# Optimization experiments

Hardware: AMD Instinct MI355X
Metric: run time of the kernel (lower is better)

Reference implementation:

```python
import jax, jax.numpy as jnp
import numpy as np

N_NODES = 1_000_000
N_EDGES = 16_000_000
N_IN, HID, N_OUT = 128, 32, 16


def setup_inputs() -> dict:
    key = jax.random.key(0)
    ks = jax.random.split(key, 8)
    x = jax.random.normal(ks[0], (N_NODES, N_IN), dtype=jnp.float32)
    edge_index = jax.random.randint(ks[1], (2, N_EDGES), 0, N_NODES, dtype=jnp.int64)
    edge_weight = jax.random.uniform(ks[2], (N_EDGES,), dtype=jnp.float32)
    # ChebConv(K=1) parameters: one linear per layer + bias
    def glorot(k, fan_in, fan_out):
        s = jnp.sqrt(6.0 / (fan_in + fan_out))
        return jax.random.uniform(k, (fan_in, fan_out), minval=-s, maxval=s, dtype=jnp.float32)
    W0 = glorot(ks[3], N_IN, HID)
    b0 = jnp.zeros((HID,), dtype=jnp.float32)
    W1 = glorot(ks[4], HID, HID)
    b1 = jnp.zeros((HID,), dtype=jnp.float32)
    W2 = glorot(ks[5], HID, N_OUT)
    b2 = jnp.zeros((N_OUT,), dtype=jnp.float32)
    return {"x": x, "edge_index": edge_index, "edge_weight": edge_weight,
            "W0": W0, "b0": b0, "W1": W1, "b1": b1, "W2": W2, "b2": b2}


def reference(x, edge_index, edge_weight, W0, b0, W1, b1, W2, b2):
    # PyG ChebConv with K=1: out = lins[0](Tx_0) + bias, Tx_0 = x.
    # The Laplacian propagation over edge_index/edge_weight is only used for K>=2,
    # so edge_index/edge_weight do not enter the math (kept for signature fidelity).
    h = jax.nn.relu(x @ W0 + b0)      # ChebConv1 + relu
    h = jax.nn.relu(h @ W1 + b1)      # ChebConv2 + relu
    # Dropout(p=0.0) is identity
    return h @ W2 + b2                # ChebConv3 -> [N, nOutputs]
```

## Files before the change

### kernel.cpp

```cpp
#include <hip/hip_runtime.h>


#define N_IN  128
#define HID   32
#define N_OUT 16

using f32x4  = __attribute__((ext_vector_type(4))) float;
using short8 = __attribute__((ext_vector_type(8))) short;
using uint4v = __attribute__((ext_vector_type(4))) unsigned int;

#define N_CHUNKS 22
#define TOTAL_WF_SHORTS (N_CHUNKS * 512)
#define WLDS_GRANULES (N_CHUNKS * 64)

__device__ __forceinline__ unsigned fu(float f) {
    union { float f; unsigned u; } v; v.f = f; return v.u;
}
__device__ __forceinline__ float uf(unsigned u) {
    union { unsigned u; float f; } v; v.u = u; return v.f;
}
__device__ __forceinline__ unsigned short f2bf_rne(float f) {
    unsigned u = fu(f);
    return (unsigned short)((u + 0x7fffu + ((u >> 16) & 1u)) >> 16);
}

__global__ void split_weights(const float* __restrict__ W0,
                              const float* __restrict__ W1,
                              const float* __restrict__ W2,
                              unsigned short* __restrict__ wf) {
    int idx = blockIdx.x * blockDim.x + threadIdx.x;
    if (idx >= TOTAL_WF_SHORTS) return;
    int chunk  = idx >> 9;
    int within = idx & 511;
    int lane = within >> 3;
    int j    = within & 7;
    const float* W; int ncol, k, col, hl;
    if (chunk < 16) {
        int kc = chunk >> 2, nh = (chunk >> 1) & 1; hl = chunk & 1;
        k = kc * 32 + 8 * (lane >> 4) + j; col = nh * 16 + (lane & 15);
        W = W0; ncol = HID;
    } else if (chunk < 20) {
        int c2 = chunk - 16, nh = c2 >> 1; hl = c2 & 1;
        k = 8 * (lane >> 4) + j; col = nh * 16 + (lane & 15);
        W = W1; ncol = HID;
    } else {
        hl = chunk - 20;
        k = 8 * (lane >> 4) + j; col = lane & 15;
        W = W2; ncol = N_OUT;
    }
    float v = W[k * ncol + col];
    unsigned hi_bits = fu(v) & 0xFFFF0000u;
    wf[idx] = (hl == 0) ? (unsigned short)(hi_bits >> 16)
                        : f2bf_rne(v - uf(hi_bits));
}

#define MFMA3(acc, ah, al, bh, bl)                                          \
    do {                                                                    \
        acc = __builtin_amdgcn_mfma_f32_16x16x32_bf16(ah, bh, acc, 0, 0, 0);\
        acc = __builtin_amdgcn_mfma_f32_16x16x32_bf16(al, bh, acc, 0, 0, 0);\
        acc = __builtin_amdgcn_mfma_f32_16x16x32_bf16(ah, bl, acc, 0, 0, 0);\
    } while (0)

__global__ __launch_bounds__(256, 4) void gnn_mfma(
    const float* __restrict__ x, const unsigned short* __restrict__ wf,
    const float* __restrict__ b0, const float* __restrict__ b1,
    const float* __restrict__ b2, float* __restrict__ out,
    int n_tiles, int stride)
{
    __shared__ __align__(16) unsigned short wlds[N_CHUNKS * 512];
    __shared__ __align__(16) unsigned short hbuf[4][2][16][40];

    const int tid  = threadIdx.x;
    const int wave = tid >> 6;
    const int l    = tid & 63;
    const int r16  = l & 15;
    const int g    = l >> 4;

    {
        const uint4v* wfv = reinterpret_cast<const uint4v*>(wf);
        uint4v* wl = reinterpret_cast<uint4v*>(wlds);
        for (int gg = tid; gg < WLDS_GRANULES; gg += 256)
            wl[gg] = wfv[gg];
    }
    __syncthreads();

    const short8* WL = reinterpret_cast<const short8*>(wlds);

    const float bc0a = b0[r16], bc0b = b0[16 + r16];
    const float bc1a = b1[r16], bc1b = b1[16 + r16];
    const float bc2  = b2[r16];

    const int gw = blockIdx.x * 4 + wave;

    for (int tile = gw; tile < n_tiles; tile += stride) {
        const int nb = tile * 16;

        f32x4 acc0 = {0.f, 0.f, 0.f, 0.f};
        f32x4 acc1 = {0.f, 0.f, 0.f, 0.f};
        const float* xrow = x + (size_t)(nb + r16) * N_IN + g * 8;

        #pragma unroll
        for (int kc = 0; kc < 4; ++kc) {
            f32x4 xa = __builtin_nontemporal_load(
                reinterpret_cast<const f32x4*>(xrow + kc * 32));
            f32x4 xb = __builtin_nontemporal_load(
                reinterpret_cast<const f32x4*>(xrow + kc * 32 + 4));
            float f[8] = {xa[0], xa[1], xa[2], xa[3], xb[0], xb[1], xb[2], xb[3]};
            uint4v hv, lv;
            #pragma unroll
            for (int p = 0; p < 4; ++p) {
                unsigned u0 = fu(f[2 * p]), u1 = fu(f[2 * p + 1]);
                unsigned h0b = u0 & 0xFFFF0000u, h1b = u1 & 0xFFFF0000u;
                hv[p] = h1b | (u0 >> 16);
                float l0 = f[2 * p] - uf(h0b), l1 = f[2 * p + 1] - uf(h1b);
                lv[p] = (fu(l1) & 0xFFFF0000u) | (fu(l0) >> 16);
            }
            short8 ah = __builtin_bit_cast(short8, hv);
            short8 al = __builtin_bit_cast(short8, lv);
            short8 w0h0 = WL[(kc * 4 + 0) * 64 + l];
            short8 w0l0 = WL[(kc * 4 + 1) * 64 + l];
            short8 w0h1 = WL[(kc * 4 + 2) * 64 + l];
            short8 w0l1 = WL[(kc * 4 + 3) * 64 + l];
            MFMA3(acc0, ah, al, w0h0, w0l0);
            MFMA3(acc1, ah, al, w0h1, w0l1);
        }

        #pragma unroll
        for (int i = 0; i < 4; ++i) {
            int row = 4 * g + i;
            float h = fmaxf(acc0[i] + bc0a, 0.f);
            unsigned hb = fu(h) & 0xFFFF0000u;
            hbuf[wave][0][row][r16] = (unsigned short)(hb >> 16);
            hbuf[wave][1][row][r16] = (unsigned short)(fu(h - uf(hb)) >> 16);
            float h2 = fmaxf(acc1[i] + bc0b, 0.f);
            unsigned hb2 = fu(h2) & 0xFFFF0000u;
            hbuf[wave][0][row][16 + r16] = (unsigned short)(hb2 >> 16);
            hbuf[wave][1][row][16 + r16] = (unsigned short)(fu(h2 - uf(hb2)) >> 16);
        }
        short8 h0h = *reinterpret_cast<const short8*>(&hbuf[wave][0][r16][g * 8]);
        short8 h0l = *reinterpret_cast<const short8*>(&hbuf[wave][1][r16][g * 8]);

        f32x4 acc2 = {0.f, 0.f, 0.f, 0.f};
        f32x4 acc3 = {0.f, 0.f, 0.f, 0.f};
        {
            short8 w1h0 = WL[(16 + 0) * 64 + l];
            short8 w1l0 = WL[(16 + 1) * 64 + l];
            short8 w1h1 = WL[(16 + 2) * 64 + l];
            short8 w1l1 = WL[(16 + 3) * 64 + l];
            MFMA3(acc2, h0h, h0l, w1h0, w1l0);
            MFMA3(acc3, h0h, h0l, w1h1, w1l1);
        }
        #pragma unroll
        for (int i = 0; i < 4; ++i) {
            int row = 4 * g + i;
            float h = fmaxf(acc2[i] + bc1a, 0.f);
            unsigned hb = fu(h) & 0xFFFF0000u;
            hbuf[wave][0][row][r16] = (unsigned short)(hb >> 16);
            hbuf[wave][1][row][r16] = (unsigned short)(fu(h - uf(hb)) >> 16);
            float h2 = fmaxf(acc3[i] + bc1b, 0.f);
            unsigned hb2 = fu(h2) & 0xFFFF0000u;
            hbuf[wave][0][row][16 + r16] = (unsigned short)(hb2 >> 16);
            hbuf[wave][1][row][16 + r16] = (unsigned short)(fu(h2 - uf(hb2)) >> 16);
        }
        short8 h1h = *reinterpret_cast<const short8*>(&hbuf[wave][0][r16][g * 8]);
        short8 h1l = *reinterpret_cast<const short8*>(&hbuf[wave][1][r16][g * 8]);

        f32x4 accO = {0.f, 0.f, 0.f, 0.f};
        {
            short8 w2h = WL[(20) * 64 + l];
            short8 w2l = WL[(21) * 64 + l];
            MFMA3(accO, h1h, h1l, w2h, w2l);
        }
        #pragma unroll
        for (int i = 0; i < 4; ++i) {
            int row = 4 * g + i;
            __builtin_nontemporal_store(
                accO[i] + bc2, out + (size_t)(nb + row) * N_OUT + r16);
        }
    }
}

extern "C" void kernel_launch(void* const* d_in, const int* in_sizes, int n_in,
                              void* d_out, int out_size, void* d_ws, size_t ws_size,
                              hipStream_t stream) {
    const float* x  = (const float*)d_in[0];
    const float* W0 = (const float*)d_in[3];
    const float* b0 = (const float*)d_in[4];
    const float* W1 = (const float*)d_in[5];
    const float* b1 = (const float*)d_in[6];
    const float* W2 = (const float*)d_in[7];
    const float* b2 = (const float*)d_in[8];
    float* out = (float*)d_out;
    unsigned short* wf = (unsigned short*)d_ws;

    int n_nodes = in_sizes[0] / N_IN;
    int n_tiles = n_nodes / 16;

    split_weights<<<(TOTAL_WF_SHORTS + 255) / 256, 256, 0, stream>>>(W0, W1, W2, wf);

    const int n_blocks = 1024;
    const int n_waves_total = n_blocks * 4;
    gnn_mfma<<<dim3(n_blocks), dim3(256), 0, stream>>>(
        x, wf, b0, b1, b2, out, n_tiles, n_waves_total);
}
```

Measured before the change: 118.7 us.

## Process two 16-row subtiles per wave to raise memory-level parallelism

Each wave now handles 32 nodes per iteration as two independent 16-row subtiles. It issues twice as many nontemporal x loads per k-chunk and shares each LDS weight fragment read across both subtiles. The aim is more memory requests in flight and fewer LDS reads per node on a kernel dominated by streaming x. In exchange, register pressure rises, so launch bounds drop to 3 waves-per-SIMD occupancy and the grid shrinks from 1024 to 768 blocks.

```diff
diff --git a/kernel.cpp b/kernel.cpp
--- a/kernel.cpp
+++ b/kernel.cpp
@@ -61,7 +61,43 @@
         acc = __builtin_amdgcn_mfma_f32_16x16x32_bf16(ah, bl, acc, 0, 0, 0);\
     } while (0)
 
-__global__ __launch_bounds__(256, 4) void gnn_mfma(
+#define SPLIT8(xa, xb, AH, AL)                                              \
+    do {                                                                    \
+        float f_[8] = {(xa)[0], (xa)[1], (xa)[2], (xa)[3],                  \
+                       (xb)[0], (xb)[1], (xb)[2], (xb)[3]};                 \
+        uint4v hv_, lv_;                                                    \
+        _Pragma("unroll")                                                   \
+        for (int p_ = 0; p_ < 4; ++p_) {                                    \
+            unsigned u0_ = fu(f_[2 * p_]), u1_ = fu(f_[2 * p_ + 1]);        \
+            unsigned h0_ = u0_ & 0xFFFF0000u, h1_ = u1_ & 0xFFFF0000u;      \
+            hv_[p_] = h1_ | (u0_ >> 16);                                    \
+            float l0_ = f_[2 * p_] - uf(h0_);                               \
+            float l1_ = f_[2 * p_ + 1] - uf(h1_);                           \
+            lv_[p_] = (fu(l1_) & 0xFFFF0000u) | (fu(l0_) >> 16);            \
+        }                                                                   \
+        AH = __builtin_bit_cast(short8, hv_);                               \
+        AL = __builtin_bit_cast(short8, lv_);                               \
+    } while (0)
+
+#define TRX(accLo, accHi, bcLo, bcHi, OUTH, OUTL)                           \
+    do {                                                                    \
+        _Pragma("unroll")                                                   \
+        for (int i_ = 0; i_ < 4; ++i_) {                                    \
+            int row_ = 4 * g + i_;                                          \
+            float h_ = fmaxf((accLo)[i_] + (bcLo), 0.f);                    \
+            unsigned hb_ = fu(h_) & 0xFFFF0000u;                            \
+            hbuf[wave][0][row_][r16] = (unsigned short)(hb_ >> 16);         \
+            hbuf[wave][1][row_][r16] = (unsigned short)(fu(h_ - uf(hb_)) >> 16); \
+            float h2_ = fmaxf((accHi)[i_] + (bcHi), 0.f);                   \
+            unsigned hb2_ = fu(h2_) & 0xFFFF0000u;                          \
+            hbuf[wave][0][row_][16 + r16] = (unsigned short)(hb2_ >> 16);   \
+            hbuf[wave][1][row_][16 + r16] = (unsigned short)(fu(h2_ - uf(hb2_)) >> 16); \
+        }                                                                   \
+        OUTH = *reinterpret_cast<const short8*>(&hbuf[wave][0][r16][g * 8]);\
+        OUTL = *reinterpret_cast<const short8*>(&hbuf[wave][1][r16][g * 8]);\
+    } while (0)
+
+__global__ __launch_bounds__(256, 3) void gnn_mfma(
     const float* __restrict__ x, const unsigned short* __restrict__ wf,
     const float* __restrict__ b0, const float* __restrict__ b1,
     const float* __restrict__ b2, float* __restrict__ out,
@@ -93,89 +129,75 @@
     const int gw = blockIdx.x * 4 + wave;
 
     for (int tile = gw; tile < n_tiles; tile += stride) {
-        const int nb = tile * 16;
-
-        f32x4 acc0 = {0.f, 0.f, 0.f, 0.f};
-        f32x4 acc1 = {0.f, 0.f, 0.f, 0.f};
-        const float* xrow = x + (size_t)(nb + r16) * N_IN + g * 8;
+        const int nb = tile * 32;
+        const float* xr0 = x + (size_t)(nb + r16) * N_IN + g * 8;
+        const float* xr1 = xr0 + (size_t)16 * N_IN;
+
+        f32x4 aA0 = {0.f, 0.f, 0.f, 0.f};
+        f32x4 aA1 = {0.f, 0.f, 0.f, 0.f};
+        f32x4 aB0 = {0.f, 0.f, 0.f, 0.f};
+        f32x4 aB1 = {0.f, 0.f, 0.f, 0.f};
 
         #pragma unroll
         for (int kc = 0; kc < 4; ++kc) {
-            f32x4 xa = __builtin_nontemporal_load(
-                reinterpret_cast<const f32x4*>(xrow + kc * 32));
-            f32x4 xb = __builtin_nontemporal_load(
-                reinterpret_cast<const f32x4*>(xrow + kc * 32 + 4));
-            float f[8] = {xa[0], xa[1], xa[2], xa[3], xb[0], xb[1], xb[2], xb[3]};
-            uint4v hv, lv;
-            #pragma unroll
-            for (int p = 0; p < 4; ++p) {
-                unsigned u0 = fu(f[2 * p]), u1 = fu(f[2 * p + 1]);
-                unsigned h0b = u0 & 0xFFFF0000u, h1b = u1 & 0xFFFF0000u;
-                hv[p] = h1b | (u0 >> 16);
-                float l0 = f[2 * p] - uf(h0b), l1 = f[2 * p + 1] - uf(h1b);
-                lv[p] = (fu(l1) & 0xFFFF0000u) | (fu(l0) >> 16);
-            }
-            short8 ah = __builtin_bit_cast(short8, hv);
-            short8 al = __builtin_bit_cast(short8, lv);
-            short8 w0h0 = WL[(kc * 4 + 0) * 64 + l];
-            short8 w0l0 = WL[(kc * 4 + 1) * 64 + l];
-            short8 w0h1 = WL[(kc * 4 + 2) * 64 + l];
-            short8 w0l1 = WL[(kc * 4 + 3) * 64 + l];
-            MFMA3(acc0, ah, al, w0h0, w0l0);
-            MFMA3(acc1, ah, al, w0h1, w0l1);
-        }
-
-        #pragma unroll
-        for (int i = 0; i < 4; ++i) {
-            int row = 4 * g + i;
-            float h = fmaxf(acc0[i] + bc0a, 0.f);
-            unsigned hb = fu(h) & 0xFFFF0000u;
-            hbuf[wave][0][row][r16] = (unsigned short)(hb >> 16);
-            hbuf[wave][1][row][r16] = (unsigned short)(fu(h - uf(hb)) >> 16);
-            float h2 = fmaxf(acc1[i] + bc0b, 0.f);
-            unsigned hb2 = fu(h2) & 0xFFFF0000u;
-            hbuf[wave][0][row][16 + r16] = (unsigned short)(hb2 >> 16);
-            hbuf[wave][1][row][16 + r16] = (unsigned short)(fu(h2 - uf(hb2)) >> 16);
-        }
-        short8 h0h = *reinterpret_cast<const short8*>(&hbuf[wave][0][r16][g * 8]);
-        short8 h0l = *reinterpret_cast<const short8*>(&hbuf[wave][1][r16][g * 8]);
-
-        f32x4 acc2 = {0.f, 0.f, 0.f, 0.f};
-        f32x4 acc3 = {0.f, 0.f, 0.f, 0.f};
+            f32x4 xa0 = __builtin_nontemporal_load(
+                reinterpret_cast<const f32x4*>(xr0 + kc * 32));
+            f32x4 xb0 = __builtin_nontemporal_load(
+                reinterpret_cast<const f32x4*>(xr0 + kc * 32 + 4));
+            f32x4 xa1 = __builtin_nontemporal_load(
+                reinterpret_cast<const f32x4*>(xr1 + kc * 32));
+            f32x4 xb1 = __builtin_nontemporal_load(
+                reinterpret_cast<const f32x4*>(xr1 + kc * 32 + 4));
+            short8 ah0, al0, ah1, al1;
+            SPLIT8(xa0, xb0, ah0, al0);
+            SPLIT8(xa1, xb1, ah1, al1);
+            short8 wh0 = WL[(kc * 4 + 0) * 64 + l];
+            short8 wl0 = WL[(kc * 4 + 1) * 64 + l];
+            short8 wh1 = WL[(kc * 4 + 2) * 64 + l];
+            short8 wl1 = WL[(kc * 4 + 3) * 64 + l];
+            MFMA3(aA0, ah0, al0, wh0, wl0);
+            MFMA3(aA1, ah0, al0, wh1, wl1);
+            MFMA3(aB0, ah1, al1, wh0, wl0);
+            MFMA3(aB1, ah1, al1, wh1, wl1);
+        }
+
+        short8 h0hA, h0lA, h0hB, h0lB;
+        TRX(aA0, aA1, bc0a, bc0b, h0hA, h0lA);
+        TRX(aB0, aB1, bc0a, bc0b, h0hB, h0lB);
+
+        f32x4 c0A = {0.f, 0.f, 0.f, 0.f};
+        f32x4 c1A = {0.f, 0.f, 0.f, 0.f};
+        f32x4 c0B = {0.f, 0.f, 0.f, 0.f};
+        f32x4 c1B = {0.f, 0.f, 0.f, 0.f};
         {
             short8 w1h0 = WL[(16 + 0) * 64 + l];
             short8 w1l0 = WL[(16 + 1) * 64 + l];
             short8 w1h1 = WL[(16 + 2) * 64 + l];
             short8 w1l1 = WL[(16 + 3) * 64 + l];
-            MFMA3(acc2, h0h, h0l, w1h0, w1l0);
-            MFMA3(acc3, h0h, h0l, w1h1, w1l1);
-        }
-        #pragma unroll
-        for (int i = 0; i < 4; ++i) {
-            int row = 4 * g + i;
-            float h = fmaxf(acc2[i] + bc1a, 0.f);
-            unsigned hb = fu(h) & 0xFFFF0000u;
-            hbuf[wave][0][row][r16] = (unsigned short)(hb >> 16);
-            hbuf[wave][1][row][r16] = (unsigned short)(fu(h - uf(hb)) >> 16);
-            float h2 = fmaxf(acc3[i] + bc1b, 0.f);
-            unsigned hb2 = fu(h2) & 0xFFFF0000u;
-            hbuf[wave][0][row][16 + r16] = (unsigned short)(hb2 >> 16);
-            hbuf[wave][1][row][16 + r16] = (unsigned short)(fu(h2 - uf(hb2)) >> 16);
-        }
-        short8 h1h = *reinterpret_cast<const short8*>(&hbuf[wave][0][r16][g * 8]);
-        short8 h1l = *reinterpret_cast<const short8*>(&hbuf[wave][1][r16][g * 8]);
-
-        f32x4 accO = {0.f, 0.f, 0.f, 0.f};
+            MFMA3(c0A, h0hA, h0lA, w1h0, w1l0);
+            MFMA3(c1A, h0hA, h0lA, w1h1, w1l1);
+            MFMA3(c0B, h0hB, h0lB, w1h0, w1l0);
+            MFMA3(c1B, h0hB, h0lB, w1h1, w1l1);
+        }
+        short8 h1hA, h1lA, h1hB, h1lB;
+        TRX(c0A, c1A, bc1a, bc1b, h1hA, h1lA);
+        TRX(c0B, c1B, bc1a, bc1b, h1hB, h1lB);
+
+        f32x4 oA = {0.f, 0.f, 0.f, 0.f};
+        f32x4 oB = {0.f, 0.f, 0.f, 0.f};
         {
             short8 w2h = WL[(20) * 64 + l];
             short8 w2l = WL[(21) * 64 + l];
-            MFMA3(accO, h1h, h1l, w2h, w2l);
+            MFMA3(oA, h1hA, h1lA, w2h, w2l);
+            MFMA3(oB, h1hB, h1lB, w2h, w2l);
         }
         #pragma unroll
         for (int i = 0; i < 4; ++i) {
             int row = 4 * g + i;
             __builtin_nontemporal_store(
-                accO[i] + bc2, out + (size_t)(nb + row) * N_OUT + r16);
+                oA[i] + bc2, out + (size_t)(nb + row) * N_OUT + r16);
+            __builtin_nontemporal_store(
+                oB[i] + bc2, out + (size_t)(nb + 16 + row) * N_OUT + r16);
         }
     }
 }
@@ -194,11 +216,11 @@
     unsigned short* wf = (unsigned short*)d_ws;
 
     int n_nodes = in_sizes[0] / N_IN;
-    int n_tiles = n_nodes / 16;
+    int n_tiles = n_nodes / 32;
 
     split_weights<<<(TOTAL_WF_SHORTS + 255) / 256, 256, 0, stream>>>(W0, W1, W2, wf);
 
-    const int n_blocks = 1024;
+    const int n_blocks = 768;
     const int n_waves_total = n_blocks * 4;
     gnn_mfma<<<dim3(n_blocks), dim3(256), 0, stream>>>(
         x, wf, b0, b1, b2, out, n_tiles, n_waves_total);
```

Measured after the change: 120.5 us. No clear change (+1.5%).

## Prefetch x tiles into LDS via async global_load_lds double buffering

Applied to the files above, without the earlier changes.

Replaces direct nontemporal global loads of x with asynchronous global-to-LDS copies into a per-wave double buffer, using an XOR swizzle to avoid bank conflicts. The next tile is prefetched while the current one is computed. The grid shrinks to 256 blocks with launch bounds of one block per CU, because the LDS footprint grows to about 97 KB. This is meant to hide load latency, but it lowers wave occupancy and memory-level parallelism for a bandwidth-bound stream.

```diff
diff --git a/kernel.cpp b/kernel.cpp
--- a/kernel.cpp
+++ b/kernel.cpp
@@ -1,4 +1,5 @@
 #include <hip/hip_runtime.h>
+#include <stdint.h>
 
 
 #define N_IN  128
@@ -61,7 +62,10 @@
         acc = __builtin_amdgcn_mfma_f32_16x16x32_bf16(ah, bl, acc, 0, 0, 0);\
     } while (0)
 
-__global__ __launch_bounds__(256, 4) void gnn_mfma(
+#define GAS1(p) ((const unsigned int __attribute__((address_space(1)))*)(uintptr_t)(p))
+#define LAS3(p) ((unsigned int __attribute__((address_space(3)))*)(uintptr_t)(p))
+
+__global__ __launch_bounds__(256, 1) void gnn_mfma(
     const float* __restrict__ x, const unsigned short* __restrict__ wf,
     const float* __restrict__ b0, const float* __restrict__ b1,
     const float* __restrict__ b2, float* __restrict__ out,
@@ -69,6 +73,7 @@
 {
     __shared__ __align__(16) unsigned short wlds[N_CHUNKS * 512];
     __shared__ __align__(16) unsigned short hbuf[4][2][16][40];
+    __shared__ __align__(16) float xbuf[4][2][2048];
 
     const int tid  = threadIdx.x;
     const int wave = tid >> 6;
@@ -92,20 +97,54 @@
 
     const int gw = blockIdx.x * 4 + wave;
 
+    const int srow = l >> 5;
+    const int st   = l & 31;
+
+    #define STAGE(buf, tileidx)                                                \
+    do {                                                                       \
+        const float* sb_ = x + (size_t)(tileidx) * 16 * N_IN;                  \
+        _Pragma("unroll")                                                      \
+        for (int i_ = 0; i_ < 8; ++i_) {                                       \
+            int row_ = i_ * 2 + srow;                                          \
+            const float* src_ = sb_ + row_ * N_IN + ((st ^ row_) << 2);        \
+            float* dst_ = &xbuf[wave][buf][i_ * 256];                          \
+            __builtin_amdgcn_global_load_lds(GAS1(src_), LAS3(dst_), 16, 0, 0);\
+        }                                                                      \
+    } while (0)
+
+    int b = 0;
+    STAGE(0, gw);
+
     for (int tile = gw; tile < n_tiles; tile += stride) {
         const int nb = tile * 16;
 
+        asm volatile("s_waitcnt vmcnt(0)" ::: "memory");
+        __builtin_amdgcn_sched_barrier(0);
+
+        f32x4 xa[4], xbv[4];
+        {
+            const f32x4* rb = reinterpret_cast<const f32x4*>(&xbuf[wave][b][r16 * 128]);
+            #pragma unroll
+            for (int kc = 0; kc < 4; ++kc) {
+                int t0 = g * 2 + kc * 8;
+                xa[kc]  = rb[t0 ^ r16];
+                xbv[kc] = rb[(t0 + 1) ^ r16];
+            }
+        }
+
+        {
+            int ntt = tile + stride;
+            int pf = (ntt < n_tiles) ? ntt : tile;
+            STAGE(b ^ 1, pf);
+        }
+
         f32x4 acc0 = {0.f, 0.f, 0.f, 0.f};
         f32x4 acc1 = {0.f, 0.f, 0.f, 0.f};
-        const float* xrow = x + (size_t)(nb + r16) * N_IN + g * 8;
 
         #pragma unroll
         for (int kc = 0; kc < 4; ++kc) {
-            f32x4 xa = __builtin_nontemporal_load(
-                reinterpret_cast<const f32x4*>(xrow + kc * 32));
-            f32x4 xb = __builtin_nontemporal_load(
-                reinterpret_cast<const f32x4*>(xrow + kc * 32 + 4));
-            float f[8] = {xa[0], xa[1], xa[2], xa[3], xb[0], xb[1], xb[2], xb[3]};
+            float f[8] = {xa[kc][0], xa[kc][1], xa[kc][2], xa[kc][3],
+                          xbv[kc][0], xbv[kc][1], xbv[kc][2], xbv[kc][3]};
             uint4v hv, lv;
             #pragma unroll
             for (int p = 0; p < 4; ++p) {
@@ -177,7 +216,10 @@
             __builtin_nontemporal_store(
                 accO[i] + bc2, out + (size_t)(nb + row) * N_OUT + r16);
         }
+
+        b ^= 1;
     }
+    #undef STAGE
 }
 
 extern "C" void kernel_launch(void* const* d_in, const int* in_sizes, int n_in,
@@ -198,7 +240,7 @@
 
     split_weights<<<(TOTAL_WF_SHORTS + 255) / 256, 256, 0, stream>>>(W0, W1, W2, wf);
 
-    const int n_blocks = 1024;
+    const int n_blocks = 256;
     const int n_waves_total = n_blocks * 4;
     gnn_mfma<<<dim3(n_blocks), dim3(256), 0, stream>>>(
         x, wf, b0, b1, b2, out, n_tiles, n_waves_total);
```

New measurement: 113.6 us. 1.05x faster.
